# Kernel tuning notes

Hardware: AMD Instinct MI355X
Metric: run time of the kernel (lower is better)

Reference implementation:

```python
import jax, jax.numpy as jnp
import numpy as np

N_NODES = 100000
N_EDGES = 1600000
D_IN = 3      # node_hidden_dim
D_GCN = 128   # gcn_dim


def setup_inputs() -> dict:
    key = jax.random.key(0)
    ks = jax.random.split(key, 10)
    x = jax.random.normal(ks[0], (N_NODES, D_IN), dtype=jnp.float32)
    edge_index = jax.random.randint(ks[1], (2, N_EDGES), 0, N_NODES, dtype=jnp.int64)
    s_in = 1.0 / np.sqrt(D_IN)
    s_h = 1.0 / np.sqrt(D_GCN)
    # PyG SAGEConv: out = lin_l(mean_{j in N(i)} x_j) + lin_r(x_i); bias lives in lin_l
    Wl0 = jax.random.uniform(ks[2], (D_IN, D_GCN), jnp.float32, -s_in, s_in)
    Wr0 = jax.random.uniform(ks[3], (D_IN, D_GCN), jnp.float32, -s_in, s_in)
    b0 = jnp.zeros((D_GCN,), jnp.float32)
    Wl1 = jax.random.uniform(ks[4], (D_GCN, D_GCN), jnp.float32, -s_h, s_h)
    Wr1 = jax.random.uniform(ks[5], (D_GCN, D_GCN), jnp.float32, -s_h, s_h)
    b1 = jnp.zeros((D_GCN,), jnp.float32)
    ln_g = jnp.ones((D_GCN,), jnp.float32)
    ln_b = jnp.zeros((D_GCN,), jnp.float32)
    return {"x": x, "edge_index": edge_index, "Wl0": Wl0, "Wr0": Wr0, "b0": b0,
            "Wl1": Wl1, "Wr1": Wr1, "b1": b1, "ln_g": ln_g, "ln_b": ln_b}


def _sage(h, src, dst, n, inv_deg, Wl, Wr, b):
    # gather source features over edges, mean-reduce onto destinations
    agg = jax.ops.segment_sum(h[src], dst, num_segments=n) * inv_deg  # [N, d]
    return agg @ Wl + h @ Wr + b


def _layernorm(h, g, b, eps=1e-5):
    mu = jnp.mean(h, axis=-1, keepdims=True)
    var = jnp.mean(jnp.square(h - mu), axis=-1, keepdims=True)
    return (h - mu) * jax.lax.rsqrt(var + eps) * g + b


def reference(x, edge_index, Wl0, Wr0, b0, Wl1, Wr1, b1, ln_g, ln_b):
    n = x.shape[0]
    src, dst = edge_index[0], edge_index[1]
    deg = jax.ops.segment_sum(jnp.ones_like(src, dtype=x.dtype), dst, num_segments=n)
    inv_deg = (1.0 / jnp.maximum(deg, 1.0))[:, None]
    h = jax.nn.relu(_sage(x, src, dst, n, inv_deg, Wl0, Wr0, b0))  # dropout = id at eval
    h = _layernorm(h, ln_g, ln_b)
    h = jax.nn.relu(_sage(h, src, dst, n, inv_deg, Wl1, Wr1, b1))
    return h
```

## Files before the change

kernel.cpp:

```cpp
#include <hip/hip_runtime.h>


#define MD 44
#define CAPB 19968
#define MAXBIN 128
#define EPB 4096

#if defined(__has_builtin)
#if __has_builtin(__builtin_amdgcn_cvt_f32_fp8) && __has_builtin(__builtin_amdgcn_cvt_pk_fp8_f32)
#define HAVE_FP8 1
#else
#define HAVE_FP8 0
#endif
#else
#define HAVE_FP8 0
#endif

typedef __attribute__((ext_vector_type(8))) short short8;
typedef __attribute__((ext_vector_type(4))) float floatx4;

__device__ __forceinline__ unsigned bf16_rne(float f) {
    unsigned u = __float_as_uint(f);
    return (u + 0x7FFFu + ((u >> 16) & 1u)) >> 16;
}
__device__ __forceinline__ float bf_lo(unsigned u) { return __uint_as_float(u << 16); }
__device__ __forceinline__ float bf_hi(unsigned u) { return __uint_as_float(u & 0xFFFF0000u); }

__global__ __launch_bounds__(256) void k_binA(
        const int* __restrict__ src, const int* __restrict__ dst,
        int* __restrict__ bcurD, int* __restrict__ bcurS,
        unsigned* __restrict__ binsD, unsigned* __restrict__ binsS,
        int E, int nbin) {
    __shared__ int cntD[MAXBIN], cntS[MAXBIN];
    __shared__ int baseD[MAXBIN], baseS[MAXBIN];
    int t = threadIdx.x;
    if (t < MAXBIN) { cntD[t] = 0; cntS[t] = 0; }
    __syncthreads();

    int i0 = blockIdx.x * EPB + t * 16;
    int dd[16], ss[16], rkD[16], rkS[16];
    int m = 0;
    if (i0 + 16 <= E) {
#pragma unroll
        for (int q = 0; q < 4; q++) {
            int4 d4 = *(const int4*)&dst[i0 + q * 4];
            int4 s4 = *(const int4*)&src[i0 + q * 4];
            dd[q * 4 + 0] = d4.x; dd[q * 4 + 1] = d4.y; dd[q * 4 + 2] = d4.z; dd[q * 4 + 3] = d4.w;
            ss[q * 4 + 0] = s4.x; ss[q * 4 + 1] = s4.y; ss[q * 4 + 2] = s4.z; ss[q * 4 + 3] = s4.w;
        }
#pragma unroll
        for (int j = 0; j < 16; j++) {
            rkD[j] = atomicAdd(&cntD[dd[j] >> 10], 1);
            rkS[j] = atomicAdd(&cntS[ss[j] >> 10], 1);
        }
        m = 16;
    } else {
        for (int j = 0; i0 + j < E && j < 16; j++) {
            dd[j] = dst[i0 + j]; ss[j] = src[i0 + j];
            rkD[j] = atomicAdd(&cntD[dd[j] >> 10], 1);
            rkS[j] = atomicAdd(&cntS[ss[j] >> 10], 1);
            m++;
        }
    }
    __syncthreads();
    if (t < nbin) {
        int c = cntD[t];
        baseD[t] = (c > 0) ? atomicAdd(&bcurD[t], c) : 0;
        c = cntS[t];
        baseS[t] = (c > 0) ? atomicAdd(&bcurS[t], c) : 0;
    }
    __syncthreads();
    for (int j = 0; j < m; j++) {
        int d = dd[j], s = ss[j];
        int gD = baseD[d >> 10] + rkD[j];
        if (gD < CAPB) binsD[(size_t)(d >> 10) * CAPB + gD] =
            ((unsigned)(d & 1023) << 17) | (unsigned)s;
        int gS = baseS[s >> 10] + rkS[j];
        if (gS < CAPB) binsS[(size_t)(s >> 10) * CAPB + gS] =
            ((unsigned)(s & 1023) << 17) | (unsigned)d;
    }
}

__global__ __launch_bounds__(256) void k_binB(
        const unsigned* __restrict__ bins, const int* __restrict__ bcur,
        int* __restrict__ counts, int* __restrict__ slots, int N) {
    __shared__ int cnt[256];
    int t = threadIdx.x;
    int bin = blockIdx.x >> 2, sub = blockIdx.x & 3;
    int llo = sub << 8;
    cnt[t] = 0;
    __syncthreads();
    int total = bcur[bin];
    if (total > CAPB) total = CAPB;
    const unsigned* brow = &bins[(size_t)bin * CAPB];
    int nbase = bin << 10;
    for (int i = t; i < total; i += 1024) {
        unsigned r0 = 0, r1 = 0, r2 = 0, r3 = 0;
        bool h0 = i < total, h1 = i + 256 < total, h2 = i + 512 < total, h3 = i + 768 < total;
        if (h0) r0 = brow[i];
        if (h1) r1 = brow[i + 256];
        if (h2) r2 = brow[i + 512];
        if (h3) r3 = brow[i + 768];
#define DEP(h, rr) if (h) { int dl = (int)(rr >> 17) - llo; \
        if ((unsigned)dl < 256u) { int r = atomicAdd(&cnt[dl], 1); \
            if (r < MD) slots[(size_t)(nbase + llo + dl) * MD + r] = (int)(rr & 0x1FFFFu); } }
        DEP(h0, r0) DEP(h1, r1) DEP(h2, r2) DEP(h3, r3)
#undef DEP
    }
    __syncthreads();
    int node = nbase + llo + t;
    if (node < N) counts[node] = cnt[t];
}

__global__ __launch_bounds__(256) void k_binC(
        const unsigned* __restrict__ binsS, const int* __restrict__ bcurS,
        const float* __restrict__ x, float* __restrict__ agg, int N) {
    __shared__ float xs[3072];
    int t = threadIdx.x;
    int bin = blockIdx.x >> 3, sub = blockIdx.x & 7;
    int sbase = bin << 10;
#pragma unroll
    for (int u = 0; u < 12; u++) {
        int li = u * 256 + t;
        int gi = sbase * 3 + li;
        xs[li] = (gi < N * 3) ? x[gi] : 0.f;
    }
    __syncthreads();
    int total = bcurS[bin];
    if (total > CAPB) total = CAPB;
    const unsigned* brow = &binsS[(size_t)bin * CAPB];
    for (int i = sub * 256 + t; i < total; i += 2048) {
        unsigned r = brow[i];
        int sl = (int)(r >> 17);
        int d = (int)(r & 0x1FFFFu);
        float v0 = xs[sl * 3 + 0], v1 = xs[sl * 3 + 1], v2 = xs[sl * 3 + 2];
        atomicAdd(&agg[(size_t)d * 3 + 0], v0);
        atomicAdd(&agg[(size_t)d * 3 + 1], v1);
        atomicAdd(&agg[(size_t)d * 3 + 2], v2);
    }
}

__global__ void k_pack_w(const float* __restrict__ Wl, const float* __restrict__ Wr,
                         uint4* __restrict__ Bp) {
    int g = blockIdx.x * 256 + threadIdx.x;
    int lane = g & 63, jt = (g >> 6) & 7, s = g >> 9;
    int k0 = s * 32 + ((lane >> 4) << 3);
    int n = jt * 16 + (lane & 15);
    unsigned w[4];
#pragma unroll
    for (int p = 0; p < 4; p++) {
        int ka = k0 + 2 * p, kb = k0 + 2 * p + 1;
        float fa = (ka < 128) ? Wl[ka * 128 + n] : Wr[(ka - 128) * 128 + n];
        float fb = (kb < 128) ? Wl[kb * 128 + n] : Wr[(kb - 128) * 128 + n];
        w[p] = bf16_rne(fa) | (bf16_rne(fb) << 16);
    }
    Bp[g] = make_uint4(w[0], w[1], w[2], w[3]);
}

__global__ __launch_bounds__(256) void k_l0lite(
        const float* __restrict__ x, const float* __restrict__ agg,
        const int* __restrict__ counts,
        const float* __restrict__ Wl0, const float* __restrict__ Wr0,
        const float* __restrict__ b0,
        const float* __restrict__ ln_g, const float* __restrict__ ln_b,
        unsigned* __restrict__ h_bf, unsigned short* __restrict__ h8, int N) {
    int t = threadIdx.x;
    int wid = t >> 6, lane = t & 63;
    const float2* Wl = (const float2*)Wl0;
    const float2* Wr = (const float2*)Wr0;
    float2 wl0 = Wl[0 * 64 + lane], wl1 = Wl[1 * 64 + lane], wl2 = Wl[2 * 64 + lane];
    float2 wr0 = Wr[0 * 64 + lane], wr1 = Wr[1 * 64 + lane], wr2 = Wr[2 * 64 + lane];
    float2 bb = ((const float2*)b0)[lane];
    float2 g = ((const float2*)ln_g)[lane];
    float2 lb = ((const float2*)ln_b)[lane];
#pragma unroll
    for (int i = 0; i < 4; i++) {
        int node = blockIdx.x * 16 + wid * 4 + i;
        if (node >= N) break;
        int deg = counts[node];
        float inv = 1.0f / fmaxf((float)deg, 1.0f);
        float A0 = agg[(size_t)node * 3 + 0] * inv;
        float A1 = agg[(size_t)node * 3 + 1] * inv;
        float A2 = agg[(size_t)node * 3 + 2] * inv;
        float X0 = x[3 * node + 0], X1 = x[3 * node + 1], X2 = x[3 * node + 2];
        float2 v = bb;
        v.x += A0 * wl0.x + A1 * wl1.x + A2 * wl2.x + X0 * wr0.x + X1 * wr1.x + X2 * wr2.x;
        v.y += A0 * wl0.y + A1 * wl1.y + A2 * wl2.y + X0 * wr0.y + X1 * wr1.y + X2 * wr2.y;
        v.x = fmaxf(v.x, 0.0f); v.y = fmaxf(v.y, 0.0f);
        float s = v.x + v.y, q = v.x * v.x + v.y * v.y;
#pragma unroll
        for (int off = 32; off; off >>= 1) {
            s += __shfl_xor(s, off, 64);
            q += __shfl_xor(q, off, 64);
        }
        float mu = s * (1.0f / 128.0f);
        float var = q * (1.0f / 128.0f) - mu * mu;
        float rstd = rsqrtf(var + 1e-5f);
        float o0 = (v.x - mu) * rstd * g.x + lb.x;
        float o1 = (v.y - mu) * rstd * g.y + lb.y;
        h_bf[(size_t)node * 64 + lane] = bf16_rne(o0) | (bf16_rne(o1) << 16);
#if HAVE_FP8
        int p = __builtin_amdgcn_cvt_pk_fp8_f32(o0, o1, 0, false);
        h8[(size_t)node * 64 + lane] = (unsigned short)(p & 0xFFFF);
#endif
    }
}

__global__ __launch_bounds__(256) void k_l0fb(
        const float* __restrict__ x, const int* __restrict__ counts,
        const int* __restrict__ slots,
        const float* __restrict__ Wl0, const float* __restrict__ Wr0,
        const float* __restrict__ b0,
        const float* __restrict__ ln_g, const float* __restrict__ ln_b,
        unsigned* __restrict__ h_bf, int N) {
    __shared__ float sagg[16][8];
    int t = threadIdx.x;
    int grp = t >> 4, sub = t & 15;
    int gnode = blockIdx.x * 16 + grp;
    float a0 = 0, a1 = 0, a2 = 0;
    if (gnode < N) {
        int deg = counts[gnode];
        int dr = min(deg, MD);
        for (int k = sub; k < dr; k += 16) {
            int s = slots[(size_t)gnode * MD + k];
            a0 += x[3 * s + 0];
            a1 += x[3 * s + 1];
            a2 += x[3 * s + 2];
        }
#pragma unroll
        for (int off = 8; off; off >>= 1) {
            a0 += __shfl_xor(a0, off, 16);
            a1 += __shfl_xor(a1, off, 16);
            a2 += __shfl_xor(a2, off, 16);
        }
        if (sub == 0) {
            float inv = 1.0f / fmaxf((float)deg, 1.0f);
            sagg[grp][0] = a0 * inv;
            sagg[grp][1] = a1 * inv;
            sagg[grp][2] = a2 * inv;
            sagg[grp][3] = x[3 * gnode + 0];
            sagg[grp][4] = x[3 * gnode + 1];
            sagg[grp][5] = x[3 * gnode + 2];
        }
    }
    __syncthreads();
    int wid = t >> 6, lane = t & 63;
    const float2* Wl = (const float2*)Wl0;
    const float2* Wr = (const float2*)Wr0;
    float2 wl0 = Wl[0 * 64 + lane], wl1 = Wl[1 * 64 + lane], wl2 = Wl[2 * 64 + lane];
    float2 wr0 = Wr[0 * 64 + lane], wr1 = Wr[1 * 64 + lane], wr2 = Wr[2 * 64 + lane];
    float2 bb = ((const float2*)b0)[lane];
    float2 g = ((const float2*)ln_g)[lane];
    float2 lb = ((const float2*)ln_b)[lane];
#pragma unroll
    for (int i = 0; i < 4; i++) {
        int nl = wid * 4 + i;
        int node = blockIdx.x * 16 + nl;
        if (node >= N) break;
        float A0 = sagg[nl][0], A1 = sagg[nl][1], A2 = sagg[nl][2];
        float X0 = sagg[nl][3], X1 = sagg[nl][4], X2 = sagg[nl][5];
        float2 v = bb;
        v.x += A0 * wl0.x + A1 * wl1.x + A2 * wl2.x + X0 * wr0.x + X1 * wr1.x + X2 * wr2.x;
        v.y += A0 * wl0.y + A1 * wl1.y + A2 * wl2.y + X0 * wr0.y + X1 * wr1.y + X2 * wr2.y;
        v.x = fmaxf(v.x, 0.0f); v.y = fmaxf(v.y, 0.0f);
        float s = v.x + v.y, q = v.x * v.x + v.y * v.y;
#pragma unroll
        for (int off = 32; off; off >>= 1) {
            s += __shfl_xor(s, off, 64);
            q += __shfl_xor(q, off, 64);
        }
        float mu = s * (1.0f / 128.0f);
        float var = q * (1.0f / 128.0f) - mu * mu;
        float rstd = rsqrtf(var + 1e-5f);
        float o0 = (v.x - mu) * rstd * g.x + lb.x;
        float o1 = (v.y - mu) * rstd * g.y + lb.y;
        h_bf[(size_t)node * 64 + lane] = bf16_rne(o0) | (bf16_rne(o1) << 16);
    }
}

#define NB 32
#define ROWU 132
template <int U8>
__global__ __launch_bounds__(256) void k_l1f(
        const uint4* __restrict__ Bp, const float* __restrict__ b1,
        const int* __restrict__ counts, const int* __restrict__ slots,
        const unsigned* __restrict__ h_bf, const unsigned short* __restrict__ h8,
        float* __restrict__ out, int N) {
    __shared__ unsigned As[NB * ROWU];
    __shared__ __align__(16) unsigned char stg[4][4096];
    __shared__ int sslot[4][8 * MD];
    int wid = threadIdx.x >> 6, lane = threadIdx.x & 63;
    int nbase = blockIdx.x * NB;

    {
        const int* sp = &slots[(size_t)(nbase + wid * 8) * MD];
#pragma unroll
        for (int u = 0; u < 5; u++) sslot[wid][u * 64 + lane] = sp[u * 64 + lane];
        if (lane < 32) sslot[wid][320 + lane] = sp[320 + lane];
    }

    const int CAP = U8 ? 32 : 16;
    for (int i = 0; i < 8; i++) {
        int nl = wid * 8 + i;
        int node = nbase + nl;
        unsigned aggw = 0, ownw = 0;
        if (node < N) {
            int deg = counts[node];
            int dr = min(deg, MD);
            float inv = 1.0f / fmaxf((float)deg, 1.0f);
            ownw = h_bf[(size_t)node * 64 + lane];
            float a0 = 0.f, a1 = 0.f;
            for (int rb = 0; rb < dr; rb += CAP) {
                int re = min(dr - rb, CAP);
#if HAVE_FP8
                if (U8) {
                    int nin = (re + 7) >> 3;
                    for (int c = 0; c < nin; c++) {
                        int ei = rb + c * 8 + (lane >> 3);
                        int s = (ei < dr) ? (sslot[wid][i * MD + ei] & 0x1FFFF) : 0;
                        const unsigned char* gp = (const unsigned char*)h8
                              + ((size_t)s * 128 + (lane & 7) * 16);
                        __builtin_amdgcn_global_load_lds(
                            (const __attribute__((address_space(1))) unsigned*)gp,
                            (__attribute__((address_space(3))) unsigned*)&stg[wid][c * 1024],
                            16, 0, 0);
                    }
                } else
#endif
                {
                    int nin = (re + 3) >> 2;
                    for (int c = 0; c < nin; c++) {
                        int ei = rb + c * 4 + (lane >> 4);
                        int s = (ei < dr) ? (sslot[wid][i * MD + ei] & 0x1FFFF) : 0;
                        const unsigned char* gp = (const unsigned char*)h_bf
                              + ((size_t)s * 256 + (lane & 15) * 16);
                        __builtin_amdgcn_global_load_lds(
                            (const __attribute__((address_space(1))) unsigned*)gp,
                            (__attribute__((address_space(3))) unsigned*)&stg[wid][c * 1024],
                            16, 0, 0);
                    }
                }
                asm volatile("s_waitcnt vmcnt(0)" ::: "memory");
                __builtin_amdgcn_sched_barrier(0);
#if HAVE_FP8
                if (U8) {
                    const unsigned short* sb = (const unsigned short*)stg[wid];
                    int r = 0;
                    for (; r + 4 <= re; r += 4) {
                        unsigned v0 = sb[(r + 0) * 64 + lane];
                        unsigned v1 = sb[(r + 1) * 64 + lane];
                        unsigned v2 = sb[(r + 2) * 64 + lane];
                        unsigned v3 = sb[(r + 3) * 64 + lane];
                        a0 += (__builtin_amdgcn_cvt_f32_fp8(v0, 0) + __builtin_amdgcn_cvt_f32_fp8(v1, 0))
                            + (__builtin_amdgcn_cvt_f32_fp8(v2, 0) + __builtin_amdgcn_cvt_f32_fp8(v3, 0));
                        a1 += (__builtin_amdgcn_cvt_f32_fp8(v0, 1) + __builtin_amdgcn_cvt_f32_fp8(v1, 1))
                            + (__builtin_amdgcn_cvt_f32_fp8(v2, 1) + __builtin_amdgcn_cvt_f32_fp8(v3, 1));
                    }
                    for (; r < re; r++) {
                        unsigned v = sb[r * 64 + lane];
                        a0 += __builtin_amdgcn_cvt_f32_fp8(v, 0);
                        a1 += __builtin_amdgcn_cvt_f32_fp8(v, 1);
                    }
                } else
#endif
                {
                    const unsigned* sb = (const unsigned*)stg[wid];
                    int r = 0;
                    for (; r + 4 <= re; r += 4) {
                        unsigned v0 = sb[(r + 0) * 64 + lane];
                        unsigned v1 = sb[(r + 1) * 64 + lane];
                        unsigned v2 = sb[(r + 2) * 64 + lane];
                        unsigned v3 = sb[(r + 3) * 64 + lane];
                        a0 += (bf_lo(v0) + bf_lo(v1)) + (bf_lo(v2) + bf_lo(v3));
                        a1 += (bf_hi(v0) + bf_hi(v1)) + (bf_hi(v2) + bf_hi(v3));
                    }
                    for (; r < re; r++) {
                        unsigned v = sb[r * 64 + lane];
                        a0 += bf_lo(v);
                        a1 += bf_hi(v);
                    }
                }
                __builtin_amdgcn_sched_barrier(0);
            }
            aggw = bf16_rne(a0 * inv) | (bf16_rne(a1 * inv) << 16);
        }
        As[nl * ROWU + lane] = aggw;
        As[nl * ROWU + 64 + lane] = ownw;
    }
    __syncthreads();

    int tile = wid >> 1;
    int jh = wid & 1;
    floatx4 acc[4];
#pragma unroll
    for (int jt = 0; jt < 4; jt++) acc[jt] = (floatx4)0.f;
    int arow = tile * 16 + (lane & 15);
    int kq = lane >> 4;
#pragma unroll
    for (int s = 0; s < 8; s++) {
        short8 af = *(const short8*)&As[arow * ROWU + s * 16 + kq * 4];
#pragma unroll
        for (int jt = 0; jt < 4; jt++) {
            short8 bf = ((const short8*)Bp)[(s * 8 + jh * 4 + jt) * 64 + lane];
            acc[jt] = __builtin_amdgcn_mfma_f32_16x16x32_bf16(af, bf, acc[jt], 0, 0, 0);
        }
    }

    int col0 = lane & 15;
#pragma unroll
    for (int r = 0; r < 4; r++) {
        int node = nbase + tile * 16 + (lane >> 4) * 4 + r;
        if (node < N) {
#pragma unroll
            for (int jt = 0; jt < 4; jt++) {
                int col = (jh * 4 + jt) * 16 + col0;
                out[(size_t)node * 128 + col] = fmaxf(acc[jt][r] + b1[col], 0.f);
            }
        }
    }
}

extern "C" void kernel_launch(void* const* d_in, const int* in_sizes, int n_in,
                              void* d_out, int out_size, void* d_ws, size_t ws_size,
                              hipStream_t stream) {
    const float* x    = (const float*)d_in[0];
    const int*   ei   = (const int*)d_in[1];
    const float* Wl0  = (const float*)d_in[2];
    const float* Wr0  = (const float*)d_in[3];
    const float* b0   = (const float*)d_in[4];
    const float* Wl1  = (const float*)d_in[5];
    const float* Wr1  = (const float*)d_in[6];
    const float* b1   = (const float*)d_in[7];
    const float* ln_g = (const float*)d_in[8];
    const float* ln_b = (const float*)d_in[9];
    float* out = (float*)d_out;

    const int N = in_sizes[0] / 3;
    const int E = in_sizes[1] / 2;
    const int* src = ei;
    const int* dst = ei + E;
    const int nbin = (N + 1023) >> 10;
    const size_t binsz = (size_t)nbin * CAPB * 4;
    const size_t region2 = ((size_t)N * 256 > 2 * binsz)
                         ? (size_t)N * 256 : 2 * binsz;

    char* base = (char*)d_ws;
    uint4* Bp   = (uint4*)base;
    int* counts = (int*)(base + 65536);
    int* bcurD  = counts + N;
    int* bcurS  = bcurD + MAXBIN;

    size_t hdr = 65536 + (size_t)N * 4 + 2 * MAXBIN * 4;
    size_t new_need = hdr + (size_t)N * 12 + (size_t)N * MD * 4 + region2 + (size_t)N * 128;
    int use_new = 0;
#if HAVE_FP8
    if (ws_size >= new_need) use_new = 1;
#endif

    float* agg      = (float*)(base + hdr);
    int* slots      = (int*)(base + hdr + (use_new ? (size_t)N * 12 : 0));
    char* reg2      = (char*)slots + (size_t)N * MD * 4;
    unsigned* binsD = (unsigned*)reg2;
    unsigned* binsS = (unsigned*)(reg2 + binsz);
    unsigned* h_bf  = (unsigned*)reg2;
    unsigned short* h8 = (unsigned short*)(reg2 + region2);

    size_t zsz = (size_t)N * 4 + 2 * MAXBIN * 4 + (use_new ? (size_t)N * 12 : 0);
    hipMemsetAsync(counts, 0, zsz, stream);
    k_pack_w<<<16, 256, 0, stream>>>(Wl1, Wr1, Bp);
    k_binA<<<(E + EPB - 1) / EPB, 256, 0, stream>>>(src, dst, bcurD, bcurS,
                                                    binsD, binsS, E, nbin);
    if (use_new)
        k_binC<<<nbin * 8, 256, 0, stream>>>(binsS, bcurS, x, agg, N);
    k_binB<<<nbin * 4, 256, 0, stream>>>(binsD, bcurD, counts, slots, N);
    if (use_new) {
        k_l0lite<<<(N + 15) / 16, 256, 0, stream>>>(x, agg, counts,
                                                    Wl0, Wr0, b0, ln_g, ln_b,
                                                    h_bf, h8, N);
        k_l1f<1><<<(N + NB - 1) / NB, 256, 0, stream>>>(Bp, b1, counts, slots,
                                                        h_bf, h8, out, N);
    } else {
        k_l0fb<<<(N + 15) / 16, 256, 0, stream>>>(x, counts, slots,
                                                  Wl0, Wr0, b0, ln_g, ln_b, h_bf, N);
        k_l1f<0><<<(N + NB - 1) / NB, 256, 0, stream>>>(Bp, b1, counts, slots,
                                                        h_bf, h8, out, N);
    }
}
```

Measured before the change: 241.4 us.

## Drop source-keyed bins; aggregate layer-0 from destination bins in shared memory

The binning kernel now writes only destination-keyed bins, which halves its scatter traffic and removes the second bin array. A new aggregation kernel gives each block one destination bin and a range of source sub-bins. It counting-sorts that bin's edges by source sub-bin in shared memory, stages each source sub-bin's x values, and accumulates into a shared per-destination buffer. Each block then flushes its nonzero totals with one global atomic per value, replacing per-edge global atomics. In exchange every block rereads its whole destination bin twice, and the shared sort buffer (SCAP) can overflow and silently drop edges if a destination bin holds many edges from one source range.

```diff
diff --git a/kernel.cpp b/kernel.cpp
--- a/kernel.cpp
+++ b/kernel.cpp
@@ -5,6 +5,9 @@
 #define CAPB 19968
 #define MAXBIN 128
 #define EPB 4096
+#define RNG 7
+#define SBR 14
+#define SCAP 3584
 
 #if defined(__has_builtin)
 #if __has_builtin(__builtin_amdgcn_cvt_f32_fp8) && __has_builtin(__builtin_amdgcn_cvt_pk_fp8_f32)
@@ -28,56 +31,51 @@
 
 __global__ __launch_bounds__(256) void k_binA(
         const int* __restrict__ src, const int* __restrict__ dst,
-        int* __restrict__ bcurD, int* __restrict__ bcurS,
-        unsigned* __restrict__ binsD, unsigned* __restrict__ binsS,
-        int E, int nbin) {
-    __shared__ int cntD[MAXBIN], cntS[MAXBIN];
-    __shared__ int baseD[MAXBIN], baseS[MAXBIN];
+        int* __restrict__ bcur, unsigned* __restrict__ bins, int E, int nbin) {
+    __shared__ int cnt[MAXBIN];
+    __shared__ int base[MAXBIN];
     int t = threadIdx.x;
-    if (t < MAXBIN) { cntD[t] = 0; cntS[t] = 0; }
+    if (t < MAXBIN) cnt[t] = 0;
     __syncthreads();
 
     int i0 = blockIdx.x * EPB + t * 16;
-    int dd[16], ss[16], rkD[16], rkS[16];
+    unsigned rec[16];
+    int bn[16], rk[16];
     int m = 0;
     if (i0 + 16 <= E) {
 #pragma unroll
         for (int q = 0; q < 4; q++) {
             int4 d4 = *(const int4*)&dst[i0 + q * 4];
             int4 s4 = *(const int4*)&src[i0 + q * 4];
-            dd[q * 4 + 0] = d4.x; dd[q * 4 + 1] = d4.y; dd[q * 4 + 2] = d4.z; dd[q * 4 + 3] = d4.w;
-            ss[q * 4 + 0] = s4.x; ss[q * 4 + 1] = s4.y; ss[q * 4 + 2] = s4.z; ss[q * 4 + 3] = s4.w;
-        }
-#pragma unroll
-        for (int j = 0; j < 16; j++) {
-            rkD[j] = atomicAdd(&cntD[dd[j] >> 10], 1);
-            rkS[j] = atomicAdd(&cntS[ss[j] >> 10], 1);
+            int dd[4] = {d4.x, d4.y, d4.z, d4.w};
+            int ss[4] = {s4.x, s4.y, s4.z, s4.w};
+#pragma unroll
+            for (int j = 0; j < 4; j++) {
+                int idx = q * 4 + j;
+                bn[idx] = dd[j] >> 10;
+                rec[idx] = ((unsigned)(dd[j] & 1023) << 17) | (unsigned)ss[j];
+                rk[idx] = atomicAdd(&cnt[bn[idx]], 1);
+            }
         }
         m = 16;
     } else {
         for (int j = 0; i0 + j < E && j < 16; j++) {
-            dd[j] = dst[i0 + j]; ss[j] = src[i0 + j];
-            rkD[j] = atomicAdd(&cntD[dd[j] >> 10], 1);
-            rkS[j] = atomicAdd(&cntS[ss[j] >> 10], 1);
+            int d = dst[i0 + j], s = src[i0 + j];
+            bn[j] = d >> 10;
+            rec[j] = ((unsigned)(d & 1023) << 17) | (unsigned)s;
+            rk[j] = atomicAdd(&cnt[bn[j]], 1);
             m++;
         }
     }
     __syncthreads();
     if (t < nbin) {
-        int c = cntD[t];
-        baseD[t] = (c > 0) ? atomicAdd(&bcurD[t], c) : 0;
-        c = cntS[t];
-        baseS[t] = (c > 0) ? atomicAdd(&bcurS[t], c) : 0;
+        int c = cnt[t];
+        base[t] = (c > 0) ? atomicAdd(&bcur[t], c) : 0;
     }
     __syncthreads();
     for (int j = 0; j < m; j++) {
-        int d = dd[j], s = ss[j];
-        int gD = baseD[d >> 10] + rkD[j];
-        if (gD < CAPB) binsD[(size_t)(d >> 10) * CAPB + gD] =
-            ((unsigned)(d & 1023) << 17) | (unsigned)s;
-        int gS = baseS[s >> 10] + rkS[j];
-        if (gS < CAPB) binsS[(size_t)(s >> 10) * CAPB + gS] =
-            ((unsigned)(s & 1023) << 17) | (unsigned)d;
+        int g = base[bn[j]] + rk[j];
+        if (g < CAPB) bins[(size_t)bn[j] * CAPB + g] = rec[j];
     }
 }
 
@@ -112,31 +110,74 @@
     if (node < N) counts[node] = cnt[t];
 }
 
-__global__ __launch_bounds__(256) void k_binC(
-        const unsigned* __restrict__ binsS, const int* __restrict__ bcurS,
-        const float* __restrict__ x, float* __restrict__ agg, int N) {
+__global__ __launch_bounds__(256) void k_binAgg(
+        const unsigned* __restrict__ bins, const int* __restrict__ bcur,
+        const float* __restrict__ x, float* __restrict__ aggS, int N, int nbin) {
+    __shared__ unsigned srt[SCAP];
     __shared__ float xs[3072];
+    __shared__ float aggL[3072];
+    __shared__ int hist[SBR], basev[SBR], rkc[SBR];
     int t = threadIdx.x;
-    int bin = blockIdx.x >> 3, sub = blockIdx.x & 7;
-    int sbase = bin << 10;
-#pragma unroll
-    for (int u = 0; u < 12; u++) {
-        int li = u * 256 + t;
-        int gi = sbase * 3 + li;
-        xs[li] = (gi < N * 3) ? x[gi] : 0.f;
-    }
-    __syncthreads();
-    int total = bcurS[bin];
+    int bin = blockIdx.x / RNG, rg = blockIdx.x % RNG;
+    int sb0 = rg * SBR;
+    if (t < SBR) { hist[t] = 0; rkc[t] = 0; }
+    for (int i = t; i < 3072; i += 256) aggL[i] = 0.f;
+    __syncthreads();
+    int total = bcur[bin];
     if (total > CAPB) total = CAPB;
-    const unsigned* brow = &binsS[(size_t)bin * CAPB];
-    for (int i = sub * 256 + t; i < total; i += 2048) {
+    const unsigned* brow = &bins[(size_t)bin * CAPB];
+    for (int i = t; i < total; i += 256) {
+        int sb = (int)((brow[i] & 0x1FFFFu) >> 10) - sb0;
+        if ((unsigned)sb < (unsigned)SBR) atomicAdd(&hist[sb], 1);
+    }
+    __syncthreads();
+    if (t == 0) {
+        int acc = 0;
+        for (int k = 0; k < SBR; k++) { basev[k] = acc; acc += hist[k]; }
+    }
+    __syncthreads();
+    for (int i = t; i < total; i += 256) {
         unsigned r = brow[i];
-        int sl = (int)(r >> 17);
-        int d = (int)(r & 0x1FFFFu);
-        float v0 = xs[sl * 3 + 0], v1 = xs[sl * 3 + 1], v2 = xs[sl * 3 + 2];
-        atomicAdd(&agg[(size_t)d * 3 + 0], v0);
-        atomicAdd(&agg[(size_t)d * 3 + 1], v1);
-        atomicAdd(&agg[(size_t)d * 3 + 2], v2);
+        int src = (int)(r & 0x1FFFFu);
+        int sb = (src >> 10) - sb0;
+        if ((unsigned)sb < (unsigned)SBR) {
+            int idx = basev[sb] + atomicAdd(&rkc[sb], 1);
+            if (idx < SCAP)
+                srt[idx] = ((unsigned)sb << 20) | ((unsigned)(src & 1023) << 10)
+                         | (r >> 17);
+        }
+    }
+    __syncthreads();
+    for (int sb = 0; sb < SBR; sb++) {
+        if (hist[sb] > 0) {
+            int sbase3 = (sb0 + sb) * 1024 * 3;
+            for (int i = t; i < 3072; i += 256) {
+                int gi = sbase3 + i;
+                xs[i] = (gi < N * 3) ? x[gi] : 0.f;
+            }
+        }
+        __syncthreads();
+        if (hist[sb] > 0) {
+            int lo = basev[sb];
+            int hi = lo + hist[sb];
+            if (hi > SCAP) hi = SCAP;
+            for (int i = lo + t; i < hi; i += 256) {
+                unsigned e = srt[i];
+                int sl = (int)((e >> 10) & 1023);
+                int dl = (int)(e & 1023);
+                atomicAdd(&aggL[dl * 3 + 0], xs[sl * 3 + 0]);
+                atomicAdd(&aggL[dl * 3 + 1], xs[sl * 3 + 1]);
+                atomicAdd(&aggL[dl * 3 + 2], xs[sl * 3 + 2]);
+            }
+        }
+        __syncthreads();
+    }
+    int nb3 = bin * 1024 * 3;
+    for (int i = t; i < 3072; i += 256) {
+        if ((nb3 + i) < N * 3) {
+            float v = aggL[i];
+            if (v != 0.f) atomicAdd(&aggS[nb3 + i], v);
+        }
     }
 }
 
@@ -441,40 +482,38 @@
     const int* dst = ei + E;
     const int nbin = (N + 1023) >> 10;
     const size_t binsz = (size_t)nbin * CAPB * 4;
-    const size_t region2 = ((size_t)N * 256 > 2 * binsz)
-                         ? (size_t)N * 256 : 2 * binsz;
+    const size_t region2 = ((size_t)N * 256 > binsz)
+                         ? (size_t)N * 256 : binsz;
 
     char* base = (char*)d_ws;
     uint4* Bp   = (uint4*)base;
     int* counts = (int*)(base + 65536);
-    int* bcurD  = counts + N;
-    int* bcurS  = bcurD + MAXBIN;
-
-    size_t hdr = 65536 + (size_t)N * 4 + 2 * MAXBIN * 4;
-    size_t new_need = hdr + (size_t)N * 12 + (size_t)N * MD * 4 + region2 + (size_t)N * 128;
+    int* bcur   = counts + N;
+
+    size_t hdr = 65536 + (size_t)N * 4 + MAXBIN * 4;
+    size_t new_need = hdr + (size_t)N * 12 + (size_t)N * MD * 4 + region2
+                    + (size_t)N * 128;
     int use_new = 0;
 #if HAVE_FP8
     if (ws_size >= new_need) use_new = 1;
 #endif
 
-    float* agg      = (float*)(base + hdr);
+    float* aggS     = (float*)(base + hdr);
     int* slots      = (int*)(base + hdr + (use_new ? (size_t)N * 12 : 0));
     char* reg2      = (char*)slots + (size_t)N * MD * 4;
     unsigned* binsD = (unsigned*)reg2;
-    unsigned* binsS = (unsigned*)(reg2 + binsz);
     unsigned* h_bf  = (unsigned*)reg2;
     unsigned short* h8 = (unsigned short*)(reg2 + region2);
 
-    size_t zsz = (size_t)N * 4 + 2 * MAXBIN * 4 + (use_new ? (size_t)N * 12 : 0);
+    size_t zsz = (size_t)N * 4 + MAXBIN * 4 + (use_new ? (size_t)N * 12 : 0);
     hipMemsetAsync(counts, 0, zsz, stream);
     k_pack_w<<<16, 256, 0, stream>>>(Wl1, Wr1, Bp);
-    k_binA<<<(E + EPB - 1) / EPB, 256, 0, stream>>>(src, dst, bcurD, bcurS,
-                                                    binsD, binsS, E, nbin);
+    k_binA<<<(E + EPB - 1) / EPB, 256, 0, stream>>>(src, dst, bcur, binsD, E, nbin);
     if (use_new)
-        k_binC<<<nbin * 8, 256, 0, stream>>>(binsS, bcurS, x, agg, N);
-    k_binB<<<nbin * 4, 256, 0, stream>>>(binsD, bcurD, counts, slots, N);
+        k_binAgg<<<nbin * RNG, 256, 0, stream>>>(binsD, bcur, x, aggS, N, nbin);
+    k_binB<<<nbin * 4, 256, 0, stream>>>(binsD, bcur, counts, slots, N);
     if (use_new) {
-        k_l0lite<<<(N + 15) / 16, 256, 0, stream>>>(x, agg, counts,
+        k_l0lite<<<(N + 15) / 16, 256, 0, stream>>>(x, aggS, counts,
                                                     Wl0, Wr0, b0, ln_g, ln_b,
                                                     h_bf, h8, N);
         k_l1f<1><<<(N + NB - 1) / NB, 256, 0, stream>>>(Bp, b1, counts, slots,
```

After: 234.6 us. -2.8%, faster.

## Replace global float atomics in layer-0 aggregation with destination-binned LDS reduction

Applied to the files above, without the earlier changes.

The source-binned scatter kernel, which did three global float atomicAdds per edge, is replaced by two passes. The first re-bins edges by destination bin and stores each edge as one 64-bit record holding the source features packed as bf16. The second reduces each destination bin in shared memory with one 1024-thread block per bin and writes the aggregate out densely. This swaps contended global atomics for an extra bin write and read plus LDS atomics, at the cost of rounding the layer-0 neighbour features to bf16 and running a kernel with only about one block per bin. The fallback path also drops the unused source binning in the binning kernel.

```diff
diff --git a/kernel.cpp b/kernel.cpp
--- a/kernel.cpp
+++ b/kernel.cpp
@@ -3,6 +3,7 @@
 
 #define MD 44
 #define CAPB 19968
+#define CAPF CAPB
 #define MAXBIN 128
 #define EPB 4096
 
@@ -26,6 +27,7 @@
 __device__ __forceinline__ float bf_lo(unsigned u) { return __uint_as_float(u << 16); }
 __device__ __forceinline__ float bf_hi(unsigned u) { return __uint_as_float(u & 0xFFFF0000u); }
 
+template <int DUAL>
 __global__ __launch_bounds__(256) void k_binA(
         const int* __restrict__ src, const int* __restrict__ dst,
         int* __restrict__ bcurD, int* __restrict__ bcurS,
@@ -51,14 +53,14 @@
 #pragma unroll
         for (int j = 0; j < 16; j++) {
             rkD[j] = atomicAdd(&cntD[dd[j] >> 10], 1);
-            rkS[j] = atomicAdd(&cntS[ss[j] >> 10], 1);
+            if (DUAL) rkS[j] = atomicAdd(&cntS[ss[j] >> 10], 1);
         }
         m = 16;
     } else {
         for (int j = 0; i0 + j < E && j < 16; j++) {
             dd[j] = dst[i0 + j]; ss[j] = src[i0 + j];
             rkD[j] = atomicAdd(&cntD[dd[j] >> 10], 1);
-            rkS[j] = atomicAdd(&cntS[ss[j] >> 10], 1);
+            if (DUAL) rkS[j] = atomicAdd(&cntS[ss[j] >> 10], 1);
             m++;
         }
     }
@@ -66,8 +68,10 @@
     if (t < nbin) {
         int c = cntD[t];
         baseD[t] = (c > 0) ? atomicAdd(&bcurD[t], c) : 0;
-        c = cntS[t];
-        baseS[t] = (c > 0) ? atomicAdd(&bcurS[t], c) : 0;
+        if (DUAL) {
+            c = cntS[t];
+            baseS[t] = (c > 0) ? atomicAdd(&bcurS[t], c) : 0;
+        }
     }
     __syncthreads();
     for (int j = 0; j < m; j++) {
@@ -75,9 +79,11 @@
         int gD = baseD[d >> 10] + rkD[j];
         if (gD < CAPB) binsD[(size_t)(d >> 10) * CAPB + gD] =
             ((unsigned)(d & 1023) << 17) | (unsigned)s;
-        int gS = baseS[s >> 10] + rkS[j];
-        if (gS < CAPB) binsS[(size_t)(s >> 10) * CAPB + gS] =
-            ((unsigned)(s & 1023) << 17) | (unsigned)d;
+        if (DUAL) {
+            int gS = baseS[s >> 10] + rkS[j];
+            if (gS < CAPB) binsS[(size_t)(s >> 10) * CAPB + gS] =
+                ((unsigned)(s & 1023) << 17) | (unsigned)d;
+        }
     }
 }
 
@@ -112,32 +118,77 @@
     if (node < N) counts[node] = cnt[t];
 }
 
-__global__ __launch_bounds__(256) void k_binC(
+__global__ __launch_bounds__(256) void k_binF(
         const unsigned* __restrict__ binsS, const int* __restrict__ bcurS,
-        const float* __restrict__ x, float* __restrict__ agg, int N) {
+        const float* __restrict__ x,
+        int* __restrict__ bcurF, unsigned long long* __restrict__ binsF,
+        int N, int nbin) {
     __shared__ float xs[3072];
+    __shared__ int cnt[MAXBIN], basev[MAXBIN], rkc[MAXBIN];
     int t = threadIdx.x;
-    int bin = blockIdx.x >> 3, sub = blockIdx.x & 7;
-    int sbase = bin << 10;
+    int bin = blockIdx.x >> 2, sub = blockIdx.x & 3;
+    if (t < MAXBIN) { cnt[t] = 0; rkc[t] = 0; }
+    int sbase3 = (bin << 10) * 3;
 #pragma unroll
     for (int u = 0; u < 12; u++) {
         int li = u * 256 + t;
-        int gi = sbase * 3 + li;
+        int gi = sbase3 + li;
         xs[li] = (gi < N * 3) ? x[gi] : 0.f;
     }
     __syncthreads();
     int total = bcurS[bin];
     if (total > CAPB) total = CAPB;
+    int chunk = (total + 3) >> 2;
+    int lo = sub * chunk;
+    int hi = lo + chunk; if (hi > total) hi = total;
     const unsigned* brow = &binsS[(size_t)bin * CAPB];
-    for (int i = sub * 256 + t; i < total; i += 2048) {
+    for (int i = lo + t; i < hi; i += 256)
+        atomicAdd(&cnt[(brow[i] & 0x1FFFFu) >> 10], 1);
+    __syncthreads();
+    if (t < nbin) {
+        int c = cnt[t];
+        basev[t] = (c > 0) ? atomicAdd(&bcurF[t], c) : 0;
+    }
+    __syncthreads();
+    for (int i = lo + t; i < hi; i += 256) {
         unsigned r = brow[i];
         int sl = (int)(r >> 17);
-        int d = (int)(r & 0x1FFFFu);
-        float v0 = xs[sl * 3 + 0], v1 = xs[sl * 3 + 1], v2 = xs[sl * 3 + 2];
-        atomicAdd(&agg[(size_t)d * 3 + 0], v0);
-        atomicAdd(&agg[(size_t)d * 3 + 1], v1);
-        atomicAdd(&agg[(size_t)d * 3 + 2], v2);
-    }
+        int d  = (int)(r & 0x1FFFFu);
+        int fb = d >> 10;
+        unsigned b0 = bf16_rne(xs[sl * 3 + 0]);
+        unsigned b1 = bf16_rne(xs[sl * 3 + 1]);
+        unsigned b2 = bf16_rne(xs[sl * 3 + 2]);
+        int g = basev[fb] + atomicAdd(&rkc[fb], 1);
+        if (g < CAPF)
+            binsF[(size_t)fb * CAPF + g] =
+                ((unsigned long long)(d & 1023) << 48) |
+                ((unsigned long long)b2 << 32) |
+                ((unsigned long long)b1 << 16) | (unsigned long long)b0;
+    }
+}
+
+__global__ __launch_bounds__(1024) void k_binD(
+        const unsigned long long* __restrict__ binsF, const int* __restrict__ bcurF,
+        float* __restrict__ aggS, int N) {
+    __shared__ float aggL[3072];
+    int t = threadIdx.x;
+    int bin = blockIdx.x;
+    for (int i = t; i < 3072; i += 1024) aggL[i] = 0.f;
+    __syncthreads();
+    int total = bcurF[bin];
+    if (total > CAPF) total = CAPF;
+    const unsigned long long* brow = &binsF[(size_t)bin * CAPF];
+    for (int i = t; i < total; i += 1024) {
+        unsigned long long e = brow[i];
+        int dl = (int)(e >> 48) & 1023;
+        atomicAdd(&aggL[dl * 3 + 0], bf_lo((unsigned)(e & 0xFFFFu)));
+        atomicAdd(&aggL[dl * 3 + 1], bf_lo((unsigned)((e >> 16) & 0xFFFFu)));
+        atomicAdd(&aggL[dl * 3 + 2], bf_lo((unsigned)((e >> 32) & 0xFFFFu)));
+    }
+    __syncthreads();
+    int nb3 = bin * 3072;
+    for (int i = t; i < 3072; i += 1024)
+        if (nb3 + i < N * 3) aggS[nb3 + i] = aggL[i];
 }
 
 __global__ void k_pack_w(const float* __restrict__ Wl, const float* __restrict__ Wr,
@@ -449,37 +500,43 @@
     int* counts = (int*)(base + 65536);
     int* bcurD  = counts + N;
     int* bcurS  = bcurD + MAXBIN;
-
-    size_t hdr = 65536 + (size_t)N * 4 + 2 * MAXBIN * 4;
-    size_t new_need = hdr + (size_t)N * 12 + (size_t)N * MD * 4 + region2 + (size_t)N * 128;
+    int* bcurF  = bcurS + MAXBIN;
+
+    size_t hdr  = 65536 + (size_t)N * 4 + 3 * MAXBIN * 4;
+    size_t aggsz = (size_t)nbin * 3072 * 4;
+    size_t new_need = hdr + aggsz + (size_t)N * MD * 4 + region2 + (size_t)N * 128;
     int use_new = 0;
 #if HAVE_FP8
     if (ws_size >= new_need) use_new = 1;
 #endif
 
-    float* agg      = (float*)(base + hdr);
-    int* slots      = (int*)(base + hdr + (use_new ? (size_t)N * 12 : 0));
+    float* aggS     = (float*)(base + hdr);
+    int* slots      = (int*)(base + hdr + (use_new ? aggsz : 0));
     char* reg2      = (char*)slots + (size_t)N * MD * 4;
     unsigned* binsD = (unsigned*)reg2;
     unsigned* binsS = (unsigned*)(reg2 + binsz);
+    unsigned long long* binsF = (unsigned long long*)(reg2 + 2 * binsz);
     unsigned* h_bf  = (unsigned*)reg2;
     unsigned short* h8 = (unsigned short*)(reg2 + region2);
 
-    size_t zsz = (size_t)N * 4 + 2 * MAXBIN * 4 + (use_new ? (size_t)N * 12 : 0);
+    size_t zsz = (size_t)N * 4 + 3 * MAXBIN * 4;
     hipMemsetAsync(counts, 0, zsz, stream);
     k_pack_w<<<16, 256, 0, stream>>>(Wl1, Wr1, Bp);
-    k_binA<<<(E + EPB - 1) / EPB, 256, 0, stream>>>(src, dst, bcurD, bcurS,
-                                                    binsD, binsS, E, nbin);
-    if (use_new)
-        k_binC<<<nbin * 8, 256, 0, stream>>>(binsS, bcurS, x, agg, N);
-    k_binB<<<nbin * 4, 256, 0, stream>>>(binsD, bcurD, counts, slots, N);
     if (use_new) {
-        k_l0lite<<<(N + 15) / 16, 256, 0, stream>>>(x, agg, counts,
+        k_binA<1><<<(E + EPB - 1) / EPB, 256, 0, stream>>>(src, dst, bcurD, bcurS,
+                                                           binsD, binsS, E, nbin);
+        k_binF<<<nbin * 4, 256, 0, stream>>>(binsS, bcurS, x, bcurF, binsF, N, nbin);
+        k_binD<<<nbin, 1024, 0, stream>>>(binsF, bcurF, aggS, N);
+        k_binB<<<nbin * 4, 256, 0, stream>>>(binsD, bcurD, counts, slots, N);
+        k_l0lite<<<(N + 15) / 16, 256, 0, stream>>>(x, aggS, counts,
                                                     Wl0, Wr0, b0, ln_g, ln_b,
                                                     h_bf, h8, N);
         k_l1f<1><<<(N + NB - 1) / NB, 256, 0, stream>>>(Bp, b1, counts, slots,
                                                         h_bf, h8, out, N);
     } else {
+        k_binA<0><<<(E + EPB - 1) / EPB, 256, 0, stream>>>(src, dst, bcurD, bcurS,
+                                                           binsD, binsD, E, nbin);
+        k_binB<<<nbin * 4, 256, 0, stream>>>(binsD, bcurD, counts, slots, N);
         k_l0fb<<<(N + 15) / 16, 256, 0, stream>>>(x, counts, slots,
                                                   Wl0, Wr0, b0, ln_g, ln_b, h_bf, N);
         k_l1f<0><<<(N + NB - 1) / NB, 256, 0, stream>>>(Bp, b1, counts, slots,
```

New measurement: 234.5 us. 1.03x faster.
